# Performance work log

Hardware: AMD Instinct MI355X
Metric: run time of the kernel (lower is better)

Reference implementation:

```python
import jax, jax.numpy as jnp
import numpy as np

B, S, E, H = 16, 2048, 128, 128  # batch, seq_len, n_embd, head_dim


def setup_inputs() -> dict:
    key = jax.random.key(0)
    ks = jax.random.split(key, 6)
    init_s = 1.0 / np.sqrt(E)  # ~ torch Linear default init scale
    return {
        "q": jax.random.normal(ks[0], (B, S, E), jnp.float32),
        "k": jax.random.normal(ks[1], (B, S, E), jnp.float32),
        "v": jax.random.normal(ks[2], (B, S, E), jnp.float32),
        "Wq": jax.random.normal(ks[3], (H, E), jnp.float32) * init_s,
        "bq": jnp.zeros((H,), jnp.float32),
        "Wk": jax.random.normal(ks[4], (H, E), jnp.float32) * init_s,
        "bk": jnp.zeros((H,), jnp.float32),
        "Wv": jax.random.normal(ks[5], (H, E), jnp.float32) * init_s,
        "bv": jnp.zeros((H,), jnp.float32),
        "mask": jnp.tril(jnp.ones((S, S), jnp.float32)),  # causal mask
    }


def reference(q, k, v, Wq, bq, Wk, bk, Wv, bv, mask):
    # Linear projections: y = x @ W.T + b (torch nn.Linear convention)
    qh = q @ Wq.T + bq  # [B,S,H]
    kh = k @ Wk.T + bk  # [B,S,H]
    vh = v @ Wv.T + bv  # [B,S,H]
    d_k = kh.shape[-1]
    wei = jnp.einsum("bqd,bkd->bqk", qh, kh) * (d_k ** -0.5)  # [B,S,S]
    wei = jnp.where(mask == 0, -jnp.inf, wei)  # masked_fill(mask==0, -inf)
    attn = jax.nn.softmax(wei, axis=-1)
    return jnp.einsum("bqk,bkd->bqd", attn, vh)  # [B,S,H]
```

## Files before the change

### kernel.cpp

```cpp
#include <hip/hip_runtime.h>
#include <hip/hip_bf16.h>

#define BATCH 16
#define SEQ   2048
#define HD    128
#define TB    64
#define QB2   128
#define KB2   128
#define NTB   (SEQ/KB2)
#define PLANE ((size_t)BATCH*SEQ*HD)

typedef __attribute__((ext_vector_type(8))) short bf16x8;
typedef __attribute__((ext_vector_type(4))) float f32x4;
typedef __attribute__((ext_vector_type(2))) unsigned int u32x2;

#define MFMA(a,b,c) __builtin_amdgcn_mfma_f32_16x16x32_bf16(a,b,c,0,0,0)

__device__ __forceinline__ short f2bf(float f){
  union{float f; unsigned u;} v; v.f = f;
  unsigned r = (v.u + 0x7FFFu + ((v.u>>16)&1u))>>16;
  return (short)r;
}
__device__ __forceinline__ unsigned packbf(float lo, float hi){
  return ((unsigned)(unsigned short)f2bf(hi) << 16) | (unsigned short)f2bf(lo);
}
__device__ __forceinline__ bf16x8 pack8(f32x4 a, f32x4 b){
  bf16x8 r;
  r[0]=f2bf(a[0]); r[1]=f2bf(a[1]); r[2]=f2bf(a[2]); r[3]=f2bf(a[3]);
  r[4]=f2bf(b[0]); r[5]=f2bf(b[1]); r[6]=f2bf(b[2]); r[7]=f2bf(b[3]);
  return r;
}
__device__ __forceinline__ bf16x8 ldfrag(const float* base, size_t eo){
  const float* p = base + eo;
  return pack8(*(const f32x4*)p, *(const f32x4*)(p+4));
}

__global__ __launch_bounds__(256)
void wconv_kernel(const float* __restrict__ Wq, const float* __restrict__ Wk,
                  const float* __restrict__ Wv, short* __restrict__ wb)
{
  int i = (blockIdx.x*256 + threadIdx.x)*8;
  const float* src = (i < 16384) ? Wq : (i < 32768 ? Wk : Wv);
  int off = i & 16383;
  f32x4 a = *(const f32x4*)(src + off);
  f32x4 b = *(const f32x4*)(src + off + 4);
  *(bf16x8*)(wb + i) = pack8(a, b);
}

__global__ __launch_bounds__(256)
void proj_kernel(const float* __restrict__ q, const float* __restrict__ k,
                 const float* __restrict__ v,
                 const float* __restrict__ bq, const float* __restrict__ bk,
                 const float* __restrict__ bv,
                 const short* __restrict__ wb, short* __restrict__ ws)
{
  __shared__ __align__(16) short T[TB*136];
  __shared__ __align__(16) short VT[HD*72];

  const int z = blockIdx.y;
  const float* x  = z==0 ? q  : (z==1 ? k  : v);
  const float* bb = z==0 ? bq : (z==1 ? bk : bv);
  const short* W  = wb + (size_t)z*HD*HD;

  const int tid = threadIdx.x;
  const int w = tid>>6, l = tid&63, li = l&15, g = l>>4;
  const int bx = blockIdx.x;
  const int rowbase = bx*TB + w*16;

  bf16x8 afr[4];
  const float* xr = x + (size_t)(rowbase+li)*HD + g*8;
  #pragma unroll
  for (int ks=0; ks<4; ks++) afr[ks] = ldfrag(xr, (size_t)ks*32);

  f32x4 acc[8];
  #pragma unroll
  for (int ct=0; ct<8; ct++) acc[ct] = (f32x4){0.f,0.f,0.f,0.f};
  #pragma unroll
  for (int ct=0; ct<8; ct++){
    #pragma unroll
    for (int ks=0; ks<4; ks++){
      bf16x8 bfr = *(const bf16x8*)(W + (size_t)(ct*16+li)*HD + ks*32 + g*8);
      acc[ct] = MFMA(afr[ks], bfr, acc[ct]);
    }
  }

  const int img  = (bx>>1);
  const int half = bx & 1;

  if (z < 2){
    #pragma unroll
    for (int ct=0; ct<8; ct++){
      float bias = bb[ct*16+li];
      #pragma unroll
      for (int r=0; r<4; r++)
        T[(w*16+g*4+r)*136 + ct*16+li] = f2bf(acc[ct][r] + bias);
    }
    __syncthreads();
    if (z == 0){
      short* dst = ws + (size_t)bx*TB*HD;
      #pragma unroll
      for (int it=0; it<4; it++){
        int c = tid + it*256, row = c>>4, c8 = c&15;
        *(bf16x8*)(dst + row*HD + c8*8) = *(const bf16x8*)&T[row*136 + c8*8];
      }
    } else {
      short* dst = ws + PLANE + (size_t)img*16384;
      #pragma unroll
      for (int it=0; it<4; it++){
        int c = tid + it*256, row = c>>4, c8 = c&15;
        int r128 = half*64 + row;
        int chunk = r128*16 + (c8 ^ (r128&7));
        *(bf16x8*)(dst + chunk*8) = *(const bf16x8*)&T[row*136 + c8*8];
      }
    }
  } else {
    #pragma unroll
    for (int ct=0; ct<8; ct++){
      float bias = bb[ct*16+li];
      #pragma unroll
      for (int r=0; r<4; r++)
        VT[(ct*16+li)*72 + w*16+g*4+r] = f2bf(acc[ct][r] + bias);
    }
    __syncthreads();
    short* dst = ws + 2*PLANE + (size_t)img*16384;
    const int d = tid>>1, hf = tid&1;
    #pragma unroll
    for (int j=0; j<4; j++){
      int c8l = hf*4 + j;
      int c8g = half*8 + c8l;
      int chunk = d*16 + (c8g ^ (d&7));
      *(bf16x8*)(dst + chunk*8) = *(const bf16x8*)&VT[d*72 + c8l*8];
    }
  }
}

__global__ __launch_bounds__(512, 2)
void attn_kernel(const short* __restrict__ ws, float* __restrict__ out)
{
  __shared__ __align__(16) short KVL[2][32768];
  __shared__ __align__(16) short PL[8][16*72];

  const int bid  = blockIdx.x;
  const int xcd  = bid & 7, slot = bid >> 3;
  const int b    = xcd*2 + (slot >> 4);
  const int qt   = slot & 15;

  const int tid = threadIdx.x;
  const int w = tid>>6, l = tid&63, li = l&15, g = l>>4;

  const short* Qw    = ws;
  const short* KimgB = ws + PLANE   + (size_t)b*NTB*16384;
  const short* VimgB = ws + 2*PLANE + (size_t)b*NTB*16384;

  const size_t qbase = (size_t)b*SEQ + qt*QB2;
  short* Pw = &PL[w][0];
  const float sc = 0.088388347648318447f;

  bf16x8 qfr[4];
  #pragma unroll
  for (int ks=0; ks<4; ks++)
    qfr[ks] = *(const bf16x8*)&Qw[(qbase + w*16 + li)*HD + ks*32 + g*8];

  f32x4 oacc[8];
  #pragma unroll
  for (int dt=0; dt<8; dt++) oacc[dt] = (f32x4){0.f,0.f,0.f,0.f};
  float mreg = -1e30f, lreg = 0.f;

  bf16x8 stg[8];
  #define LOADT(kt_) do{                                                    \
    const short* sK = KimgB + (size_t)(kt_)*16384;                          \
    const short* sV = VimgB + (size_t)(kt_)*16384;                          \
    _Pragma("unroll")                                                       \
    for (int j=0;j<4;j++) stg[j]   = *(const bf16x8*)(sK + (tid + j*512)*8);\
    _Pragma("unroll")                                                       \
    for (int j=0;j<4;j++) stg[4+j] = *(const bf16x8*)(sV + (tid + j*512)*8);\
  }while(0)
  #define WRT(nb_) do{                                                     \
    short* dK = &KVL[nb_][0];                                              \
    short* dV = &KVL[nb_][16384];                                          \
    _Pragma("unroll")                                                      \
    for (int j=0;j<4;j++) *(bf16x8*)(dK + (tid+j*512)*8) = stg[j];         \
    _Pragma("unroll")                                                      \
    for (int j=0;j<4;j++) *(bf16x8*)(dV + (tid+j*512)*8) = stg[4+j];       \
  }while(0)

  LOADT(0); WRT(0); __syncthreads();
  int cur = 0;

  for (int kt=0; kt<=qt; kt++){
    const bool pre = (kt < qt);
    if (pre) LOADT(kt+1);

    const short* KL = &KVL[cur][0];
    const short* VL = &KVL[cur][16384];

    f32x4 st[8];
    #pragma unroll
    for (int ct=0; ct<8; ct++) st[ct] = (f32x4){0.f,0.f,0.f,0.f};
    #pragma unroll
    for (int ct=0; ct<8; ct++){
      const int row = ct*16 + li;
      #pragma unroll
      for (int ks=0; ks<4; ks++){
        const int chunk = row*16 + ((ks*4 + g) ^ (row&7));
        bf16x8 kfr = *(const bf16x8*)&KL[chunk*8];
        st[ct] = MFMA(kfr, qfr[ks], st[ct]);
      }
    }

    float sv[8][4];
    float pm = -1e30f;
    const bool diag = (kt == qt);
    const int qloc = w*16 + li;
    #pragma unroll
    for (int ct=0; ct<8; ct++){
      #pragma unroll
      for (int r=0; r<4; r++){
        float x = st[ct][r]*sc;
        if (diag && (ct*16 + g*4 + r) > qloc) x = -1e30f;
        sv[ct][r] = x;
        pm = fmaxf(pm, x);
      }
    }
    pm = fmaxf(pm, __shfl_xor(pm, 16));
    pm = fmaxf(pm, __shfl_xor(pm, 32));
    float mn   = fmaxf(mreg, pm);
    float sclq = __expf(mreg - mn);
    mreg = mn;
    float psum = 0.f;
    #pragma unroll
    for (int ct=0; ct<8; ct++){
      #pragma unroll
      for (int r=0; r<4; r++){
        float p = __expf(sv[ct][r] - mn);
        sv[ct][r] = p;
        psum += p;
      }
    }
    psum += __shfl_xor(psum, 16);
    psum += __shfl_xor(psum, 32);
    lreg = lreg*sclq + psum;

    float sclo[4];
    #pragma unroll
    for (int r=0; r<4; r++) sclo[r] = __shfl(sclq, g*4 + r);
    #pragma unroll
    for (int dt=0; dt<8; dt++){
      #pragma unroll
      for (int r=0; r<4; r++) oacc[dt][r] *= sclo[r];
    }

    #pragma unroll
    for (int h2=0; h2<2; h2++){
      #pragma unroll
      for (int c4=0; c4<4; c4++){
        const int ct = h2*4 + c4;
        u32x2 pw;
        pw[0] = packbf(sv[ct][0], sv[ct][1]);
        pw[1] = packbf(sv[ct][2], sv[ct][3]);
        *(u32x2*)&Pw[li*72 + c4*16 + g*4] = pw;
      }
      #pragma unroll
      for (int ks2=0; ks2<2; ks2++){
        bf16x8 afr = *(const bf16x8*)&Pw[li*72 + ks2*32 + g*8];
        #pragma unroll
        for (int dt=0; dt<8; dt++){
          const int row = dt*16 + li;
          const int c8g = h2*8 + ks2*4 + g;
          const int chunk = row*16 + (c8g ^ (row&7));
          bf16x8 bfr = *(const bf16x8*)&VL[chunk*8];
          oacc[dt] = MFMA(afr, bfr, oacc[dt]);
        }
      }
    }

    if (pre) WRT(cur^1);
    __syncthreads();
    cur ^= 1;
  }

  float lso[4];
  #pragma unroll
  for (int r=0; r<4; r++) lso[r] = __shfl(lreg, g*4 + r);
  float* Ob = out + qbase*HD;
  #pragma unroll
  for (int dt=0; dt<8; dt++){
    #pragma unroll
    for (int r=0; r<4; r++){
      Ob[(size_t)(w*16 + g*4 + r)*HD + dt*16 + li] = oacc[dt][r] / lso[r];
    }
  }
  #undef LOADT
  #undef WRT
}

extern "C" void kernel_launch(void* const* d_in, const int* in_sizes, int n_in,
                              void* d_out, int out_size, void* d_ws, size_t ws_size,
                              hipStream_t stream)
{
  short* ws = (short*)d_ws;
  short* wb = ws + 3*PLANE;

  wconv_kernel<<<24, 256, 0, stream>>>(
      (const float*)d_in[3], (const float*)d_in[5], (const float*)d_in[7], wb);

  dim3 pg(BATCH*SEQ/TB, 3);
  proj_kernel<<<pg, 256, 0, stream>>>(
      (const float*)d_in[0], (const float*)d_in[1], (const float*)d_in[2],
      (const float*)d_in[4], (const float*)d_in[6], (const float*)d_in[8],
      wb, ws);

  attn_kernel<<<dim3(BATCH*NTB), 512, 0, stream>>>(ws, (float*)d_out);
}
```

Measured before the change: 106.5 us.

## Switch attention to 32x32 MFMA with key-split waves and register-resident P

Recasts the attention inner loop to use 32x32x16 bf16 MFMA instead of 16x16x32. The 8 waves now split as 4 query groups of 32 rows times 2 key halves. P is assembled into the A-operand with cross-half shuffles instead of a round trip through LDS. The two key halves share a running max through LDS on each tile, and their partial outputs and row sums are merged through LDS at the end. This aims for denser matrix-core use and less LDS traffic for P, at the cost of an extra block-wide barrier per key tile and a final reduction step.

```diff
diff --git a/kernel.cpp b/kernel.cpp
--- a/kernel.cpp
+++ b/kernel.cpp
@@ -10,11 +10,12 @@
 #define NTB   (SEQ/KB2)
 #define PLANE ((size_t)BATCH*SEQ*HD)
 
-typedef __attribute__((ext_vector_type(8))) short bf16x8;
-typedef __attribute__((ext_vector_type(4))) float f32x4;
-typedef __attribute__((ext_vector_type(2))) unsigned int u32x2;
-
-#define MFMA(a,b,c) __builtin_amdgcn_mfma_f32_16x16x32_bf16(a,b,c,0,0,0)
+typedef __attribute__((ext_vector_type(8)))  short bf16x8;
+typedef __attribute__((ext_vector_type(4)))  float f32x4;
+typedef __attribute__((ext_vector_type(16))) float f32x16;
+
+#define MFMA(a,b,c)   __builtin_amdgcn_mfma_f32_16x16x32_bf16(a,b,c,0,0,0)
+#define MFMA32(a,b,c) __builtin_amdgcn_mfma_f32_32x32x16_bf16(a,b,c,0,0,0)
 
 __device__ __forceinline__ short f2bf(float f){
   union{float f; unsigned u;} v; v.f = f;
@@ -33,6 +34,12 @@
 __device__ __forceinline__ bf16x8 ldfrag(const float* base, size_t eo){
   const float* p = base + eo;
   return pack8(*(const f32x4*)p, *(const f32x4*)(p+4));
+}
+__device__ __forceinline__ bf16x8 mkfrag(unsigned w0, unsigned w1,
+                                         unsigned w2, unsigned w3){
+  union{ unsigned u[4]; bf16x8 v; } t;
+  t.u[0]=w0; t.u[1]=w1; t.u[2]=w2; t.u[3]=w3;
+  return t.v;
 }
 
 __global__ __launch_bounds__(256)
@@ -138,7 +145,8 @@
 void attn_kernel(const short* __restrict__ ws, float* __restrict__ out)
 {
   __shared__ __align__(16) short KVL[2][32768];
-  __shared__ __align__(16) short PL[8][16*72];
+  __shared__ float sm[4][2][2][32];
+  __shared__ float scl_l[4][2][32];
 
   const int bid  = blockIdx.x;
   const int xcd  = bid & 7, slot = bid >> 3;
@@ -146,25 +154,27 @@
   const int qt   = slot & 15;
 
   const int tid = threadIdx.x;
-  const int w = tid>>6, l = tid&63, li = l&15, g = l>>4;
+  const int w = tid>>6, l = tid&63;
+  const int s = w & 3, h = w >> 2;
+  const int lq = l & 31, h5 = l >> 5;
 
   const short* Qw    = ws;
   const short* KimgB = ws + PLANE   + (size_t)b*NTB*16384;
   const short* VimgB = ws + 2*PLANE + (size_t)b*NTB*16384;
 
   const size_t qbase = (size_t)b*SEQ + qt*QB2;
-  short* Pw = &PL[w][0];
   const float sc = 0.088388347648318447f;
-
-  bf16x8 qfr[4];
-  #pragma unroll
-  for (int ks=0; ks<4; ks++)
-    qfr[ks] = *(const bf16x8*)&Qw[(qbase + w*16 + li)*HD + ks*32 + g*8];
-
-  f32x4 oacc[8];
-  #pragma unroll
-  for (int dt=0; dt<8; dt++) oacc[dt] = (f32x4){0.f,0.f,0.f,0.f};
-  float mreg = -1e30f, lreg = 0.f;
+  const int qg = (int)(qt*QB2) + s*32 + lq;
+
+  bf16x8 qfr[8];
+  #pragma unroll
+  for (int ks=0; ks<8; ks++)
+    qfr[ks] = *(const bf16x8*)&Qw[(qbase + s*32 + lq)*HD + ks*16 + h5*8];
+
+  f32x16 oacc[4];
+  #pragma unroll
+  for (int db=0; db<4; db++) oacc[db] = (f32x16)(0.f);
+  float m_run = -1e30f, l_run = 0.f;
 
   bf16x8 stg[8];
   #define LOADT(kt_) do{                                                    \
@@ -194,82 +204,99 @@
     const short* KL = &KVL[cur][0];
     const short* VL = &KVL[cur][16384];
 
-    f32x4 st[8];
-    #pragma unroll
-    for (int ct=0; ct<8; ct++) st[ct] = (f32x4){0.f,0.f,0.f,0.f};
-    #pragma unroll
-    for (int ct=0; ct<8; ct++){
-      const int row = ct*16 + li;
-      #pragma unroll
-      for (int ks=0; ks<4; ks++){
-        const int chunk = row*16 + ((ks*4 + g) ^ (row&7));
+    f32x16 sacc[2];
+    sacc[0] = (f32x16)(0.f); sacc[1] = (f32x16)(0.f);
+    #pragma unroll
+    for (int ct=0; ct<2; ct++){
+      const int r = h*64 + ct*32 + lq;
+      #pragma unroll
+      for (int ks=0; ks<8; ks++){
+        const int chunk = r*16 + ((2*ks + h5) ^ (r&7));
         bf16x8 kfr = *(const bf16x8*)&KL[chunk*8];
-        st[ct] = MFMA(kfr, qfr[ks], st[ct]);
-      }
-    }
-
-    float sv[8][4];
+        sacc[ct] = MFMA32(kfr, qfr[ks], sacc[ct]);
+      }
+    }
+
+    float sv[2][16];
     float pm = -1e30f;
     const bool diag = (kt == qt);
-    const int qloc = w*16 + li;
-    #pragma unroll
-    for (int ct=0; ct<8; ct++){
-      #pragma unroll
-      for (int r=0; r<4; r++){
-        float x = st[ct][r]*sc;
-        if (diag && (ct*16 + g*4 + r) > qloc) x = -1e30f;
+    #pragma unroll
+    for (int ct=0; ct<2; ct++){
+      #pragma unroll
+      for (int r=0; r<16; r++){
+        float x = sacc[ct][r]*sc;
+        if (diag){
+          int k_loc = h*64 + ct*32 + (r&3) + 8*(r>>2) + 4*h5;
+          if (kt*KB2 + k_loc > qg - (int)(qt*QB2) + (int)(qt*KB2)) x = -1e30f;
+        }
         sv[ct][r] = x;
         pm = fmaxf(pm, x);
       }
     }
-    pm = fmaxf(pm, __shfl_xor(pm, 16));
     pm = fmaxf(pm, __shfl_xor(pm, 32));
-    float mn   = fmaxf(mreg, pm);
-    float sclq = __expf(mreg - mn);
-    mreg = mn;
     float psum = 0.f;
     #pragma unroll
-    for (int ct=0; ct<8; ct++){
-      #pragma unroll
-      for (int r=0; r<4; r++){
-        float p = __expf(sv[ct][r] - mn);
+    for (int ct=0; ct<2; ct++){
+      #pragma unroll
+      for (int r=0; r<16; r++){
+        float p = __expf(sv[ct][r] - pm);
         sv[ct][r] = p;
         psum += p;
       }
     }
-    psum += __shfl_xor(psum, 16);
     psum += __shfl_xor(psum, 32);
-    lreg = lreg*sclq + psum;
-
-    float sclo[4];
-    #pragma unroll
-    for (int r=0; r<4; r++) sclo[r] = __shfl(sclq, g*4 + r);
-    #pragma unroll
-    for (int dt=0; dt<8; dt++){
-      #pragma unroll
-      for (int r=0; r<4; r++) oacc[dt][r] *= sclo[r];
-    }
-
-    #pragma unroll
-    for (int h2=0; h2<2; h2++){
-      #pragma unroll
-      for (int c4=0; c4<4; c4++){
-        const int ct = h2*4 + c4;
-        u32x2 pw;
-        pw[0] = packbf(sv[ct][0], sv[ct][1]);
-        pw[1] = packbf(sv[ct][2], sv[ct][3]);
-        *(u32x2*)&Pw[li*72 + c4*16 + g*4] = pw;
-      }
-      #pragma unroll
-      for (int ks2=0; ks2<2; ks2++){
-        bf16x8 afr = *(const bf16x8*)&Pw[li*72 + ks2*32 + g*8];
+
+    if (l < 32){ sm[s][h][0][lq] = pm; sm[s][h][1][lq] = psum; }
+    __syncthreads();
+    float pm_p = sm[s][h^1][0][lq];
+    float ps_p = sm[s][h^1][1][lq];
+    float m_new  = fmaxf(m_run, fmaxf(pm, pm_p));
+    float sclq   = __expf(m_run - m_new);
+    float pscale = __expf(pm - m_new);
+    m_run = m_new;
+    l_run = l_run*sclq + psum*pscale;
+    (void)ps_p;
+    if (l < 32) scl_l[s][h][lq] = sclq;
+
+    float sclr[16];
+    #pragma unroll
+    for (int r=0; r<16; r++)
+      sclr[r] = scl_l[s][h][(r&3) + 8*(r>>2) + 4*h5];
+    #pragma unroll
+    for (int db=0; db<4; db++){
+      #pragma unroll
+      for (int r=0; r<16; r++) oacc[db][r] *= sclr[r];
+    }
+
+    #pragma unroll
+    for (int ct=0; ct<2; ct++){
+      unsigned G[4][2], GX[4][2];
+      #pragma unroll
+      for (int g2=0; g2<4; g2++){
         #pragma unroll
-        for (int dt=0; dt<8; dt++){
-          const int row = dt*16 + li;
-          const int c8g = h2*8 + ks2*4 + g;
-          const int chunk = row*16 + (c8g ^ (row&7));
-          bf16x8 bfr = *(const bf16x8*)&VL[chunk*8];
-          oacc[dt] = MFMA(afr, bfr, oacc[dt]);
+        for (int p=0; p<2; p++)
+          G[g2][p] = packbf(sv[ct][g2*4+2*p]*pscale, sv[ct][g2*4+2*p+1]*pscale);
+      }
+      #pragma unroll
+      for (int g2=0; g2<4; g2++){
+        #pragma unroll
+        for (int p=0; p<2; p++)
+          GX[g2][p] = __shfl_xor((int)G[g2][p], 32);
+      }
+      bf16x8 pf0 = h5 ? mkfrag(GX[1][0],GX[1][1],G[1][0],G[1][1])
+                      : mkfrag(G[0][0],G[0][1],GX[0][0],GX[0][1]);
+      bf16x8 pf1 = h5 ? mkfrag(GX[3][0],GX[3][1],G[3][0],G[3][1])
+                      : mkfrag(G[2][0],G[2][1],GX[2][0],GX[2][1]);
+      #pragma unroll
+      for (int ksp=0; ksp<2; ksp++){
+        bf16x8 pf = ksp ? pf1 : pf0;
+        #pragma unroll
+        for (int db=0; db<4; db++){
+          const int d = db*32 + lq;
+          const int c8 = h*8 + ct*4 + ksp*2 + h5;
+          const int chunk = d*16 + (c8 ^ (d&7));
+          bf16x8 vfr = *(const bf16x8*)&VL[chunk*8];
+          oacc[db] = MFMA32(pf, vfr, oacc[db]);
         }
       }
     }
@@ -279,15 +306,34 @@
     cur ^= 1;
   }
 
-  float lso[4];
-  #pragma unroll
-  for (int r=0; r<4; r++) lso[r] = __shfl(lreg, g*4 + r);
-  float* Ob = out + qbase*HD;
-  #pragma unroll
-  for (int dt=0; dt<8; dt++){
-    #pragma unroll
-    for (int r=0; r<4; r++){
-      Ob[(size_t)(w*16 + g*4 + r)*HD + dt*16 + li] = oacc[dt][r] / lso[r];
+  if (l < 32) sm[s][h][1][lq] = l_run;
+  float* Obuf = (float*)&KVL[0][0];
+  if (h == 1){
+    #pragma unroll
+    for (int db=0; db<4; db++){
+      #pragma unroll
+      for (int r=0; r<16; r++){
+        int qr = (r&3) + 8*(r>>2) + 4*h5;
+        Obuf[s*4096 + qr*128 + db*32 + lq] = oacc[db][r];
+      }
+    }
+  }
+  __syncthreads();
+  if (h == 0){
+    float lt[16];
+    #pragma unroll
+    for (int r=0; r<16; r++){
+      int qr = (r&3) + 8*(r>>2) + 4*h5;
+      lt[r] = sm[s][0][1][qr] + sm[s][1][1][qr];
+    }
+    #pragma unroll
+    for (int db=0; db<4; db++){
+      #pragma unroll
+      for (int r=0; r<16; r++){
+        int qr = (r&3) + 8*(r>>2) + 4*h5;
+        float o = (oacc[db][r] + Obuf[s*4096 + qr*128 + db*32 + lq]) / lt[r];
+        out[(qbase + s*32 + qr)*HD + db*32 + lq] = o;
+      }
     }
   }
   #undef LOADT
```

Result: no change. 108.0 us (+1.4%).

## Shrink attention tiles to 64x64 with 256-thread blocks and balanced causal scheduling

Applied to the files above, without the earlier changes.

Attention query and key tiles shrink from 128 to 64 rows, blocks go from 8 waves to 4, and the grid doubles to 512 blocks. K/V tiles are now read as halves of the existing 128-row swizzled images, with a new index for the V half. Block slots are mapped so query tiles run in mirrored order, which spreads causal work more evenly across the batch, and MFMA sections are wrapped in s_setprio. The goal is better occupancy and load balance for the triangular workload, at the cost of more K/V reloads per query row and more loop iterations.

```diff
diff --git a/kernel.cpp b/kernel.cpp
--- a/kernel.cpp
+++ b/kernel.cpp
@@ -5,9 +5,9 @@
 #define SEQ   2048
 #define HD    128
 #define TB    64
-#define QB2   128
-#define KB2   128
-#define NTB   (SEQ/KB2)
+#define QB3   64
+#define KB3   64
+#define NT3   (SEQ/QB3)
 #define PLANE ((size_t)BATCH*SEQ*HD)
 
 typedef __attribute__((ext_vector_type(8))) short bf16x8;
@@ -134,25 +134,26 @@
   }
 }
 
-__global__ __launch_bounds__(512, 2)
+__global__ __launch_bounds__(256, 2)
 void attn_kernel(const short* __restrict__ ws, float* __restrict__ out)
 {
-  __shared__ __align__(16) short KVL[2][32768];
-  __shared__ __align__(16) short PL[8][16*72];
+  __shared__ __align__(16) short KVL[2][16384];
+  __shared__ __align__(16) short PL[4][16*72];
 
   const int bid  = blockIdx.x;
   const int xcd  = bid & 7, slot = bid >> 3;
-  const int b    = xcd*2 + (slot >> 4);
-  const int qt   = slot & 15;
+  const int b    = xcd*2 + (slot >> 5);
+  const int sl   = slot & 31;
+  const int qt   = (slot < 32) ? sl : (31 - sl);
 
   const int tid = threadIdx.x;
   const int w = tid>>6, l = tid&63, li = l&15, g = l>>4;
 
   const short* Qw    = ws;
-  const short* KimgB = ws + PLANE   + (size_t)b*NTB*16384;
-  const short* VimgB = ws + 2*PLANE + (size_t)b*NTB*16384;
-
-  const size_t qbase = (size_t)b*SEQ + qt*QB2;
+  const short* KimgB = ws + PLANE   + (size_t)b*(SEQ/128)*16384;
+  const short* VimgB = ws + 2*PLANE + (size_t)b*(SEQ/128)*16384;
+
+  const size_t qbase = (size_t)b*SEQ + qt*QB3;
   short* Pw = &PL[w][0];
   const float sc = 0.088388347648318447f;
 
@@ -167,21 +168,25 @@
   float mreg = -1e30f, lreg = 0.f;
 
   bf16x8 stg[8];
-  #define LOADT(kt_) do{                                                    \
-    const short* sK = KimgB + (size_t)(kt_)*16384;                          \
-    const short* sV = VimgB + (size_t)(kt_)*16384;                          \
+  #define LOADT(kt_) do{                                                     \
+    const short* sK = KimgB + (size_t)((kt_)>>1)*16384 + ((kt_)&1)*8192;     \
+    const short* sV = VimgB + (size_t)((kt_)>>1)*16384;                      \
+    const int vh = ((kt_)&1)*8;                                              \
+    _Pragma("unroll")                                                        \
+    for (int j=0;j<4;j++) stg[j] = *(const bf16x8*)(sK + (tid + j*256)*8);   \
+    _Pragma("unroll")                                                        \
+    for (int j=0;j<4;j++){                                                   \
+      int i = tid + j*256, d = i>>3, c8s = i&7;                              \
+      stg[4+j] = *(const bf16x8*)(sV + (d*16 + vh + c8s)*8);                 \
+    }                                                                        \
+  }while(0)
+  #define WRT(nb_) do{                                                      \
+    short* dK = &KVL[nb_][0];                                               \
+    short* dV = &KVL[nb_][8192];                                            \
     _Pragma("unroll")                                                       \
-    for (int j=0;j<4;j++) stg[j]   = *(const bf16x8*)(sK + (tid + j*512)*8);\
+    for (int j=0;j<4;j++) *(bf16x8*)(dK + (tid+j*256)*8) = stg[j];          \
     _Pragma("unroll")                                                       \
-    for (int j=0;j<4;j++) stg[4+j] = *(const bf16x8*)(sV + (tid + j*512)*8);\
-  }while(0)
-  #define WRT(nb_) do{                                                     \
-    short* dK = &KVL[nb_][0];                                              \
-    short* dV = &KVL[nb_][16384];                                          \
-    _Pragma("unroll")                                                      \
-    for (int j=0;j<4;j++) *(bf16x8*)(dK + (tid+j*512)*8) = stg[j];         \
-    _Pragma("unroll")                                                      \
-    for (int j=0;j<4;j++) *(bf16x8*)(dV + (tid+j*512)*8) = stg[4+j];       \
+    for (int j=0;j<4;j++) *(bf16x8*)(dV + (tid+j*256)*8) = stg[4+j];        \
   }while(0)
 
   LOADT(0); WRT(0); __syncthreads();
@@ -192,13 +197,14 @@
     if (pre) LOADT(kt+1);
 
     const short* KL = &KVL[cur][0];
-    const short* VL = &KVL[cur][16384];
-
-    f32x4 st[8];
-    #pragma unroll
-    for (int ct=0; ct<8; ct++) st[ct] = (f32x4){0.f,0.f,0.f,0.f};
-    #pragma unroll
-    for (int ct=0; ct<8; ct++){
+    const short* VL = &KVL[cur][8192];
+
+    f32x4 st[4];
+    #pragma unroll
+    for (int ct=0; ct<4; ct++) st[ct] = (f32x4){0.f,0.f,0.f,0.f};
+    __builtin_amdgcn_s_setprio(1);
+    #pragma unroll
+    for (int ct=0; ct<4; ct++){
       const int row = ct*16 + li;
       #pragma unroll
       for (int ks=0; ks<4; ks++){
@@ -207,13 +213,14 @@
         st[ct] = MFMA(kfr, qfr[ks], st[ct]);
       }
     }
-
-    float sv[8][4];
+    __builtin_amdgcn_s_setprio(0);
+
+    float sv[4][4];
     float pm = -1e30f;
     const bool diag = (kt == qt);
     const int qloc = w*16 + li;
     #pragma unroll
-    for (int ct=0; ct<8; ct++){
+    for (int ct=0; ct<4; ct++){
       #pragma unroll
       for (int r=0; r<4; r++){
         float x = st[ct][r]*sc;
@@ -229,7 +236,7 @@
     mreg = mn;
     float psum = 0.f;
     #pragma unroll
-    for (int ct=0; ct<8; ct++){
+    for (int ct=0; ct<4; ct++){
       #pragma unroll
       for (int r=0; r<4; r++){
         float p = __expf(sv[ct][r] - mn);
@@ -251,28 +258,25 @@
     }
 
     #pragma unroll
-    for (int h2=0; h2<2; h2++){
-      #pragma unroll
-      for (int c4=0; c4<4; c4++){
-        const int ct = h2*4 + c4;
-        u32x2 pw;
-        pw[0] = packbf(sv[ct][0], sv[ct][1]);
-        pw[1] = packbf(sv[ct][2], sv[ct][3]);
-        *(u32x2*)&Pw[li*72 + c4*16 + g*4] = pw;
-      }
-      #pragma unroll
-      for (int ks2=0; ks2<2; ks2++){
-        bf16x8 afr = *(const bf16x8*)&Pw[li*72 + ks2*32 + g*8];
-        #pragma unroll
-        for (int dt=0; dt<8; dt++){
-          const int row = dt*16 + li;
-          const int c8g = h2*8 + ks2*4 + g;
-          const int chunk = row*16 + (c8g ^ (row&7));
-          bf16x8 bfr = *(const bf16x8*)&VL[chunk*8];
-          oacc[dt] = MFMA(afr, bfr, oacc[dt]);
-        }
-      }
-    }
+    for (int c4=0; c4<4; c4++){
+      u32x2 pw;
+      pw[0] = packbf(sv[c4][0], sv[c4][1]);
+      pw[1] = packbf(sv[c4][2], sv[c4][3]);
+      *(u32x2*)&Pw[li*72 + c4*16 + g*4] = pw;
+    }
+    __builtin_amdgcn_s_setprio(1);
+    #pragma unroll
+    for (int ks2=0; ks2<2; ks2++){
+      bf16x8 afr = *(const bf16x8*)&Pw[li*72 + ks2*32 + g*8];
+      #pragma unroll
+      for (int dt=0; dt<8; dt++){
+        const int d = dt*16 + li;
+        const int chunk = d*8 + ((ks2*4 + g) ^ (d&7));
+        bf16x8 bfr = *(const bf16x8*)&VL[chunk*8];
+        oacc[dt] = MFMA(afr, bfr, oacc[dt]);
+      }
+    }
+    __builtin_amdgcn_s_setprio(0);
 
     if (pre) WRT(cur^1);
     __syncthreads();
@@ -310,5 +314,5 @@
       (const float*)d_in[4], (const float*)d_in[6], (const float*)d_in[8],
       wb, ws);
 
-  attn_kernel<<<dim3(BATCH*NTB), 512, 0, stream>>>(ws, (float*)d_out);
-}
+  attn_kernel<<<dim3(BATCH*NT3), 256, 0, stream>>>(ws, (float*)d_out);
+}
```

After: 99.43 us. 1.07x faster.
